# Optimization experiments

Measured on AMD Instinct MI355X. Metric: run time of the kernel, lower is better.

The kernel has to match this reference:

```python
import jax, jax.numpy as jnp
import numpy as np

V = 1048576          # number of non-empty voxels (all batches concatenated)
P = 4                # max_num_points_per_voxel (hard-coded in module)
C_IN = 4             # INPUT_DIM (radar point features)
C_OUT = 32           # SIMPLIFIED_POINTNET.OUT_CHANNEL


def setup_inputs() -> dict:
    key = jax.random.key(0)
    k1, k2, k3 = jax.random.split(key, 3)
    voxel_features = jax.random.normal(k1, (V, P, C_IN), dtype=jnp.float32)
    W = jax.random.normal(k2, (C_OUT, C_IN), dtype=jnp.float32)
    voxel_num_points = jax.random.randint(k3, (V,), 0, 5, dtype=jnp.int64)
    return {"voxel_features": voxel_features, "W": W,
            "voxel_num_points": voxel_num_points}


def reference(voxel_features, W, voxel_num_points):
    # simplified_pointnet: Linear(C_IN -> C_OUT, bias=False), applied per point
    proj = jnp.einsum('vpc,oc->vpo', voxel_features, W)      # [V, P, C_OUT]
    # pooling == 'mean': sum over points, divide by clamped point count
    summed = proj.sum(axis=1)                                # [V, C_OUT]
    normalizer = jnp.maximum(voxel_num_points, 1).astype(summed.dtype)[:, None]
    return summed / normalizer                               # sp_features
```

## Files before the change

### kernel.cpp

```cpp
#include <hip/hip_runtime.h>


__global__ __launch_bounds__(256) void radar_pointnet_kernel(
    const float* __restrict__ feat,
    const float* __restrict__ Wm,
    const int*   __restrict__ npts,
    float*       __restrict__ out,
    int V)
{
    int t = blockIdx.x * blockDim.x + threadIdx.x;
    int v  = t >> 3;
    if (v >= V) return;
    int oc = t & 7;

    const float4* f4 = (const float4*)feat;
    size_t fb = (size_t)v * 4;
    float4 p0 = f4[fb + 0];
    float4 p1 = f4[fb + 1];
    float4 p2 = f4[fb + 2];
    float4 p3 = f4[fb + 3];
    float sx = p0.x + p1.x + p2.x + p3.x;
    float sy = p0.y + p1.y + p2.y + p3.y;
    float sz = p0.z + p1.z + p2.z + p3.z;
    float sw = p0.w + p1.w + p2.w + p3.w;

    const float4* Wf4 = (const float4*)Wm;
    int wb = oc * 4;
    float4 w0 = Wf4[wb + 0];
    float4 w1 = Wf4[wb + 1];
    float4 w2 = Wf4[wb + 2];
    float4 w3 = Wf4[wb + 3];

    int n = npts[v];
    float inv = 1.0f / (float)(n > 1 ? n : 1);

    float4 o;
    o.x = (sx * w0.x + sy * w0.y + sz * w0.z + sw * w0.w) * inv;
    o.y = (sx * w1.x + sy * w1.y + sz * w1.z + sw * w1.w) * inv;
    o.z = (sx * w2.x + sy * w2.y + sz * w2.z + sw * w2.w) * inv;
    o.w = (sx * w3.x + sy * w3.y + sz * w3.z + sw * w3.w) * inv;

    ((float4*)out)[(size_t)v * 8 + oc] = o;
}

extern "C" void kernel_launch(void* const* d_in, const int* in_sizes, int n_in,
                              void* d_out, int out_size, void* d_ws, size_t ws_size,
                              hipStream_t stream) {
    const float* feat = (const float*)d_in[0];
    const float* Wm   = (const float*)d_in[1];
    const int*   np   = (const int*)d_in[2];
    float*       out  = (float*)d_out;

    int V = in_sizes[0] / 16;
    int threads = V * 8;
    int block = 256;
    int grid = (threads + block - 1) / block;

    radar_pointnet_kernel<<<grid, block, 0, stream>>>(feat, Wm, np, out, V);
}
```

Before: 211.3 us.

## Use 4 threads per voxel with shuffle-reduced sums and a grid-stride loop

```diff
diff --git a/kernel.cpp b/kernel.cpp
--- a/kernel.cpp
+++ b/kernel.cpp
@@ -8,39 +8,44 @@
     float*       __restrict__ out,
     int V)
 {
-    int t = blockIdx.x * blockDim.x + threadIdx.x;
-    int v  = t >> 3;
-    if (v >= V) return;
-    int oc = t & 7;
+    const int tid = blockIdx.x * blockDim.x + threadIdx.x;
+    const int q   = tid & 3;
+    const int g0  = tid >> 2;
+    const int ngroups = (gridDim.x * blockDim.x) >> 2;
 
-    const float4* f4 = (const float4*)feat;
-    size_t fb = (size_t)v * 4;
-    float4 p0 = f4[fb + 0];
-    float4 p1 = f4[fb + 1];
-    float4 p2 = f4[fb + 2];
-    float4 p3 = f4[fb + 3];
-    float sx = p0.x + p1.x + p2.x + p3.x;
-    float sy = p0.y + p1.y + p2.y + p3.y;
-    float sz = p0.z + p1.z + p2.z + p3.z;
-    float sw = p0.w + p1.w + p2.w + p3.w;
+    const float4* __restrict__ Wf4 = (const float4*)Wm;
+    float4 w[8];
+#pragma unroll
+    for (int j = 0; j < 8; ++j) w[j] = Wf4[q * 8 + j];
 
-    const float4* Wf4 = (const float4*)Wm;
-    int wb = oc * 4;
-    float4 w0 = Wf4[wb + 0];
-    float4 w1 = Wf4[wb + 1];
-    float4 w2 = Wf4[wb + 2];
-    float4 w3 = Wf4[wb + 3];
+    const float4* __restrict__ f4 = (const float4*)feat;
 
-    int n = npts[v];
-    float inv = 1.0f / (float)(n > 1 ? n : 1);
+#pragma unroll 2
+    for (int v = g0; v < V; v += ngroups) {
+        float4 p = f4[(size_t)v * 4 + q];
 
-    float4 o;
-    o.x = (sx * w0.x + sy * w0.y + sz * w0.z + sw * w0.w) * inv;
-    o.y = (sx * w1.x + sy * w1.y + sz * w1.z + sw * w1.w) * inv;
-    o.z = (sx * w2.x + sy * w2.y + sz * w2.z + sw * w2.w) * inv;
-    o.w = (sx * w3.x + sy * w3.y + sz * w3.z + sw * w3.w) * inv;
+        p.x += __shfl_xor(p.x, 1); p.y += __shfl_xor(p.y, 1);
+        p.z += __shfl_xor(p.z, 1); p.w += __shfl_xor(p.w, 1);
+        p.x += __shfl_xor(p.x, 2); p.y += __shfl_xor(p.y, 2);
+        p.z += __shfl_xor(p.z, 2); p.w += __shfl_xor(p.w, 2);
 
-    ((float4*)out)[(size_t)v * 8 + oc] = o;
+        int n = npts[v];
+        float inv = 1.0f / (float)(n > 1 ? n : 1);
+
+        float4 o0, o1;
+        o0.x = (p.x*w[0].x + p.y*w[0].y + p.z*w[0].z + p.w*w[0].w) * inv;
+        o0.y = (p.x*w[1].x + p.y*w[1].y + p.z*w[1].z + p.w*w[1].w) * inv;
+        o0.z = (p.x*w[2].x + p.y*w[2].y + p.z*w[2].z + p.w*w[2].w) * inv;
+        o0.w = (p.x*w[3].x + p.y*w[3].y + p.z*w[3].z + p.w*w[3].w) * inv;
+        o1.x = (p.x*w[4].x + p.y*w[4].y + p.z*w[4].z + p.w*w[4].w) * inv;
+        o1.y = (p.x*w[5].x + p.y*w[5].y + p.z*w[5].z + p.w*w[5].w) * inv;
+        o1.z = (p.x*w[6].x + p.y*w[6].y + p.z*w[6].z + p.w*w[6].w) * inv;
+        o1.w = (p.x*w[7].x + p.y*w[7].y + p.z*w[7].z + p.w*w[7].w) * inv;
+
+        float4* __restrict__ ob = (float4*)(out + (size_t)v * 32 + q * 8);
+        ob[0] = o0;
+        ob[1] = o1;
+    }
 }
 
 extern "C" void kernel_launch(void* const* d_in, const int* in_sizes, int n_in,
@@ -52,9 +57,12 @@
     float*       out  = (float*)d_out;
 
     int V = in_sizes[0] / 16;
-    int threads = V * 8;
+
     int block = 256;
-    int grid = (threads + block - 1) / block;
+    int grid  = 2048;
+    int max_grid = (V * 4 + block - 1) / block;
+    if (grid > max_grid) grid = max_grid;
+    if (grid < 1) grid = 1;
 
     radar_pointnet_kernel<<<grid, block, 0, stream>>>(feat, Wm, np, out, V);
 }
```

Measured after the change: 197.3 us. 6.6% less time.
